# Performance work log

Hardware: AMD Instinct MI355X
Metric: run time of the kernel (lower is better)

Reference implementation:

```python
import jax, jax.numpy as jnp
import numpy as np

N = 8192      # num nodes
E = 8192      # num hyperedges
D = 256       # embedding dim
DENSITY = 0.01
LEAKY = 0.2   # negative_slope of LeakyReLU


def setup_inputs() -> dict:
    key = jax.random.key(0)
    k1, k2, k3, k4, k5 = jax.random.split(key, 5)
    # sparse adjacency matrices represented densely (values * bernoulli mask)
    inp_adj = jax.random.normal(k1, (E, N), dtype=jnp.float32) * (
        jax.random.uniform(k2, (E, N)) < DENSITY
    ).astype(jnp.float32)
    att_adj = jax.random.normal(k3, (N, E), dtype=jnp.float32) * (
        jax.random.uniform(k4, (N, E)) < DENSITY
    ).astype(jnp.float32)
    embs = jax.random.normal(k5, (N, D), dtype=jnp.float32)
    return {"inp_adj": inp_adj, "att_adj": att_adj, "embs": embs}


def reference(inp_adj, att_adj, embs):
    # adj = att_adj @ inp_adj  (spgemm in the original)  -> [N, N]
    adj = att_adj @ inp_adj
    # adj @ (adj.T @ embs)  (two spmm)  -> [N, D]
    out = adj @ (adj.T @ embs)
    # LeakyReLU(negative_slope=LEAKY)
    return jnp.where(out > 0, out, LEAKY * out)
```

## Files before the change

kernel.cpp:

```cpp
#include <hip/hip_runtime.h>
#include <stdint.h>

#define NROWS 8192
#define NCOLS 8192
#define DDIM  256
#define SLOTS 160
#define SCRN  192
#define CAP   786432

__device__ __forceinline__ float bf16lo(uint32_t u) { return __uint_as_float(u << 16); }
__device__ __forceinline__ float bf16hi(uint32_t u) { return __uint_as_float(u & 0xffff0000u); }
__device__ __forceinline__ uint32_t f2bf(float f) {
    uint32_t b = __float_as_uint(f);
    return (b + 0x7fffu + ((b >> 16) & 1u)) >> 16;
}

__global__ __launch_bounds__(256) void cvt_kernel(const float* __restrict__ in,
                                                  uint32_t* __restrict__ out) {
    int i = blockIdx.x * 256 + threadIdx.x;
    float2 f = ((const float2*)in)[i];
    out[i] = f2bf(f.x) | (f2bf(f.y) << 16);
}

__global__ __launch_bounds__(256) void zero_kernel(int* __restrict__ a,
                                                   int* __restrict__ b) {
    int i = blockIdx.x * 256 + threadIdx.x;
    a[i] = 0;
    b[i] = 0;
}

__device__ __forceinline__ void emit_nz(float v, uint32_t col, int& base,
                                        uint2* __restrict__ s) {
    unsigned long long m = __ballot(v != 0.f);
    if (m) {
        if (v != 0.f) {
            int pre = __builtin_amdgcn_mbcnt_hi((uint32_t)(m >> 32),
                      __builtin_amdgcn_mbcnt_lo((uint32_t)m, 0u));
            int o = base + pre;
            if (o < SCRN) s[o] = make_uint2(col, __float_as_uint(v));
        }
        base += (int)__popcll(m);
    }
}

template<int CH>
__device__ __forceinline__ void process_chunk(const float4 (&d)[8], int lane,
                                              int& base, uint2* __restrict__ s) {
    #pragma unroll
    for (int i = 0; i < 8; ++i) {
        const uint32_t cbase = (uint32_t)((CH * 512 + i * 64 + lane) * 4);
        emit_nz(d[i].x, cbase + 0, base, s);
        emit_nz(d[i].y, cbase + 1, base, s);
        emit_nz(d[i].z, cbase + 2, base, s);
        emit_nz(d[i].w, cbase + 3, base, s);
    }
}

__global__ __launch_bounds__(256) void extract_kernel(
        const float* __restrict__ M,
        int* __restrict__ rc, uint2* __restrict__ pair, int* __restrict__ ct) {
    __shared__ uint2 scr[4][SCRN];
    const int wv   = threadIdx.x >> 6;
    const int lane = threadIdx.x & 63;
    const int r = blockIdx.x * 4 + wv;

    const float4* __restrict__ M4 = (const float4*)(M + (size_t)r * NCOLS);
    uint2* __restrict__ dst = pair + (size_t)r * SLOTS;
    uint2* __restrict__ s = scr[wv];

    float4 da[8], db[8];
    #pragma unroll
    for (int i = 0; i < 8; ++i) da[i] = M4[0 * 512 + i * 64 + lane];
    #pragma unroll
    for (int i = 0; i < 8; ++i) db[i] = M4[1 * 512 + i * 64 + lane];
    __builtin_amdgcn_sched_barrier(0);

    int base = 0;
    process_chunk<0>(da, lane, base, s);
    #pragma unroll
    for (int i = 0; i < 8; ++i) da[i] = M4[2 * 512 + i * 64 + lane];
    __builtin_amdgcn_sched_barrier(0);
    process_chunk<1>(db, lane, base, s);
    #pragma unroll
    for (int i = 0; i < 8; ++i) db[i] = M4[3 * 512 + i * 64 + lane];
    __builtin_amdgcn_sched_barrier(0);
    process_chunk<2>(da, lane, base, s);
    process_chunk<3>(db, lane, base, s);

    const int n = base < SLOTS ? base : SLOTS;
    for (int j = lane; j < n; j += 64) {
        uint2 e = s[j];
        dst[j] = e;
        atomicAdd(&ct[e.x], 1);
    }
    if (lane == 0) rc[r] = n;
}

__global__ __launch_bounds__(256) void prefix_kernel(
        const int* __restrict__ totA, int* __restrict__ startA, int* __restrict__ curA,
        const int* __restrict__ totB, int* __restrict__ startB, int* __restrict__ curB) {
    const int* cnt = blockIdx.x ? totB : totA;
    int* start     = blockIdx.x ? startB : startA;
    int* cur       = blockIdx.x ? curB : curA;
    __shared__ int wtot[4];
    const int tid = threadIdx.x;
    const int wv = tid >> 6, lane = tid & 63;
    const int chunk = NCOLS / 256;
    const int base = tid * chunk;
    int sum = 0;
    for (int i = 0; i < chunk; ++i) sum += cnt[base + i];
    int inc = sum;
    #pragma unroll
    for (int sd = 1; sd < 64; sd <<= 1) {
        int t = __shfl_up(inc, sd, 64);
        if (lane >= sd) inc += t;
    }
    if (lane == 63) wtot[wv] = inc;
    __syncthreads();
    if (tid == 0) {
        int acc = 0;
        #pragma unroll
        for (int i = 0; i < 4; ++i) { int t = wtot[i]; wtot[i] = acc; acc += t; }
    }
    __syncthreads();
    int run = wtot[wv] + inc - sum;
    for (int i = 0; i < chunk; ++i) {
        start[base + i] = run;
        cur[base + i]   = run;
        run += cnt[base + i];
    }
}

__global__ __launch_bounds__(256) void scatter_kernel(
        const int* __restrict__ rcA, const uint2* __restrict__ pairA,
        int* __restrict__ curA, uint2* __restrict__ cscA,
        const int* __restrict__ rcB, const uint2* __restrict__ pairB,
        int* __restrict__ curB, uint2* __restrict__ cscB) {
    const int wv   = threadIdx.x >> 6;
    const int lane = threadIdx.x & 63;
    const int W = blockIdx.x * 4 + wv;
    const int which = W >> 13;
    const int r = W & (NROWS - 1);
    const uint2* pair = which ? pairB : pairA;
    int* cur          = which ? curB : curA;
    uint2* csc        = which ? cscB : cscA;
    const int c = (which ? rcB : rcA)[r];
    const uint2* __restrict__ p = pair + (size_t)r * SLOTS;
    for (int j = lane; j < c; j += 64) {
        uint2 e = p[j];
        int slot = atomicAdd(&cur[e.x], 1);
        csc[slot] = make_uint2((uint32_t)r, e.y);
    }
}

struct Acc8 { float a0, a1, a2, a3, a4, a5, a6, a7; };

__device__ __forceinline__ void fma8(Acc8& a, float v, uint4 t) {
    a.a0 = fmaf(v, bf16lo(t.x), a.a0); a.a1 = fmaf(v, bf16hi(t.x), a.a1);
    a.a2 = fmaf(v, bf16lo(t.y), a.a2); a.a3 = fmaf(v, bf16hi(t.y), a.a3);
    a.a4 = fmaf(v, bf16lo(t.z), a.a4); a.a5 = fmaf(v, bf16hi(t.z), a.a5);
    a.a6 = fmaf(v, bf16lo(t.w), a.a6); a.a7 = fmaf(v, bf16hi(t.w), a.a7);
}

template<int FINAL>
__global__ __launch_bounds__(256) void spmm_kernel(
        const int* __restrict__ start, const int* __restrict__ cnt,
        const uint2* __restrict__ pairs,
        const uint4* __restrict__ X,
        void* __restrict__ Y, int fixed_stride) {
    const int wv   = threadIdx.x >> 6;
    const int lane = threadIdx.x & 63;
    const int half = lane >> 5, sub = lane & 31;
    const int r = blockIdx.x * 4 + wv;
    const int c = cnt[r];
    const uint2* __restrict__ P = pairs + (fixed_stride ? (size_t)r * SLOTS : (size_t)start[r]);
    Acc8 a = {0.f, 0.f, 0.f, 0.f, 0.f, 0.f, 0.f, 0.f};
    int j = 0;
    const int nfull = c >> 4;
    if (nfull > 0) {
        uint2 p[8];
        #pragma unroll
        for (int t = 0; t < 8; ++t) p[t] = P[2 * t + half];
        for (int b = 0; b < nfull; ++b) {
            uint2 pn[8];
            if (b + 1 < nfull) {
                #pragma unroll
                for (int t = 0; t < 8; ++t) pn[t] = P[(b + 1) * 16 + 2 * t + half];
            }
            uint4 x[8];
            #pragma unroll
            for (int t = 0; t < 8; ++t) x[t] = X[(size_t)p[t].x * 32 + sub];
            #pragma unroll
            for (int t = 0; t < 8; ++t) fma8(a, __uint_as_float(p[t].y), x[t]);
            #pragma unroll
            for (int t = 0; t < 8; ++t) p[t] = pn[t];
        }
        j = nfull * 16;
    }
    for (; j + 1 < c; j += 2) {
        uint2 p = P[j + half];
        uint4 x = X[(size_t)p.x * 32 + sub];
        fma8(a, __uint_as_float(p.y), x);
    }
    if (j < c) {
        uint2 p = P[j];
        uint4 x = X[(size_t)p.x * 32 + sub];
        float v = half ? 0.f : __uint_as_float(p.y);
        fma8(a, v, x);
    }
    a.a0 += __shfl_xor(a.a0, 32); a.a1 += __shfl_xor(a.a1, 32);
    a.a2 += __shfl_xor(a.a2, 32); a.a3 += __shfl_xor(a.a3, 32);
    a.a4 += __shfl_xor(a.a4, 32); a.a5 += __shfl_xor(a.a5, 32);
    a.a6 += __shfl_xor(a.a6, 32); a.a7 += __shfl_xor(a.a7, 32);
    if (half == 0) {
        if (FINAL) {
            a.a0 = a.a0 > 0.f ? a.a0 : 0.2f * a.a0; a.a1 = a.a1 > 0.f ? a.a1 : 0.2f * a.a1;
            a.a2 = a.a2 > 0.f ? a.a2 : 0.2f * a.a2; a.a3 = a.a3 > 0.f ? a.a3 : 0.2f * a.a3;
            a.a4 = a.a4 > 0.f ? a.a4 : 0.2f * a.a4; a.a5 = a.a5 > 0.f ? a.a5 : 0.2f * a.a5;
            a.a6 = a.a6 > 0.f ? a.a6 : 0.2f * a.a6; a.a7 = a.a7 > 0.f ? a.a7 : 0.2f * a.a7;
            float4* Y4 = (float4*)Y;
            Y4[(size_t)r * 64 + sub * 2]     = make_float4(a.a0, a.a1, a.a2, a.a3);
            Y4[(size_t)r * 64 + sub * 2 + 1] = make_float4(a.a4, a.a5, a.a6, a.a7);
        } else {
            uint4 o;
            o.x = f2bf(a.a0) | (f2bf(a.a1) << 16);
            o.y = f2bf(a.a2) | (f2bf(a.a3) << 16);
            o.z = f2bf(a.a4) | (f2bf(a.a5) << 16);
            o.w = f2bf(a.a6) | (f2bf(a.a7) << 16);
            ((uint4*)Y)[(size_t)r * 32 + sub] = o;
        }
    }
}

extern "C" void kernel_launch(void* const* d_in, const int* in_sizes, int n_in,
                              void* d_out, int out_size, void* d_ws, size_t ws_size,
                              hipStream_t stream) {
    const float* Bm   = (const float*)d_in[0];
    const float* Am   = (const float*)d_in[1];
    const float* embs = (const float*)d_in[2];
    float* out = (float*)d_out;

    char* w = (char*)d_ws;
    auto alloc = [&](size_t bytes) -> char* {
        char* p = w;
        w += (bytes + 255) & ~(size_t)255;
        return p;
    };
    uint32_t* embs16 = (uint32_t*)alloc((size_t)NROWS * DDIM * 2);
    uint32_t* t1     = (uint32_t*)alloc((size_t)NROWS * DDIM * 2);
    uint32_t* t2     = (uint32_t*)alloc((size_t)NROWS * DDIM * 2);
    uint32_t* t3     = t1;

    int* rcA       = (int*)alloc(NROWS * 4);
    int* rcB       = (int*)alloc(NROWS * 4);
    int* coltotA   = (int*)alloc(NCOLS * 4);
    int* colstartA = (int*)alloc(NCOLS * 4);
    int* curA      = (int*)alloc(NCOLS * 4);
    int* coltotB   = (int*)alloc(NCOLS * 4);
    int* colstartB = (int*)alloc(NCOLS * 4);
    int* curB      = (int*)alloc(NCOLS * 4);

    uint2* csrA = (uint2*)alloc((size_t)NROWS * SLOTS * 8);
    uint2* csrB = (uint2*)alloc((size_t)NROWS * SLOTS * 8);
    uint2* cscA = (uint2*)alloc((size_t)CAP * 8);
    uint2* cscB = (uint2*)alloc((size_t)CAP * 8);

    zero_kernel<<<32, 256, 0, stream>>>(coltotA, coltotB);
    cvt_kernel<<<(NROWS * DDIM / 2) / 256, 256, 0, stream>>>(embs, embs16);
    extract_kernel<<<NROWS / 4, 256, 0, stream>>>(Am, rcA, csrA, coltotA);
    extract_kernel<<<NROWS / 4, 256, 0, stream>>>(Bm, rcB, csrB, coltotB);
    prefix_kernel<<<2, 256, 0, stream>>>(coltotA, colstartA, curA,
                                         coltotB, colstartB, curB);
    scatter_kernel<<<2 * NROWS / 4, 256, 0, stream>>>(rcA, csrA, curA, cscA,
                                                      rcB, csrB, curB, cscB);
    spmm_kernel<0><<<NROWS / 4, 256, 0, stream>>>(colstartA, coltotA, cscA, (const uint4*)embs16, t1, 0);
    spmm_kernel<0><<<NROWS / 4, 256, 0, stream>>>(colstartB, coltotB, cscB, (const uint4*)t1, t2, 0);
    spmm_kernel<0><<<NROWS / 4, 256, 0, stream>>>(nullptr, rcB, csrB, (const uint4*)t2, t3, 1);
    spmm_kernel<1><<<NROWS / 4, 256, 0, stream>>>(nullptr, rcA, csrA, (const uint4*)t3, out, 1);

    (void)in_sizes; (void)n_in; (void)out_size; (void)ws_size;
}
```

Measured before the change: 712.0 us.

## Fuse scatter and four SpMM stages into one persistent kernel with grid barriers

Measured after the change: 1.220 ms. +71.3%, slower.

```diff
diff --git a/kernel.cpp b/kernel.cpp
--- a/kernel.cpp
+++ b/kernel.cpp
@@ -7,6 +7,8 @@
 #define SLOTS 160
 #define SCRN  192
 #define CAP   786432
+#define MBLK  1024
+#define MWAVE (MBLK * 4)
 
 __device__ __forceinline__ float bf16lo(uint32_t u) { return __uint_as_float(u << 16); }
 __device__ __forceinline__ float bf16hi(uint32_t u) { return __uint_as_float(u & 0xffff0000u); }
@@ -23,10 +25,12 @@
 }
 
 __global__ __launch_bounds__(256) void zero_kernel(int* __restrict__ a,
-                                                   int* __restrict__ b) {
+                                                   int* __restrict__ b,
+                                                   int* __restrict__ bar) {
     int i = blockIdx.x * 256 + threadIdx.x;
     a[i] = 0;
     b[i] = 0;
+    if (i == 0) bar[0] = 0;
 }
 
 __device__ __forceinline__ void emit_nz(float v, uint32_t col, int& base,
@@ -131,28 +135,6 @@
     }
 }
 
-__global__ __launch_bounds__(256) void scatter_kernel(
-        const int* __restrict__ rcA, const uint2* __restrict__ pairA,
-        int* __restrict__ curA, uint2* __restrict__ cscA,
-        const int* __restrict__ rcB, const uint2* __restrict__ pairB,
-        int* __restrict__ curB, uint2* __restrict__ cscB) {
-    const int wv   = threadIdx.x >> 6;
-    const int lane = threadIdx.x & 63;
-    const int W = blockIdx.x * 4 + wv;
-    const int which = W >> 13;
-    const int r = W & (NROWS - 1);
-    const uint2* pair = which ? pairB : pairA;
-    int* cur          = which ? curB : curA;
-    uint2* csc        = which ? cscB : cscA;
-    const int c = (which ? rcB : rcA)[r];
-    const uint2* __restrict__ p = pair + (size_t)r * SLOTS;
-    for (int j = lane; j < c; j += 64) {
-        uint2 e = p[j];
-        int slot = atomicAdd(&cur[e.x], 1);
-        csc[slot] = make_uint2((uint32_t)r, e.y);
-    }
-}
-
 struct Acc8 { float a0, a1, a2, a3, a4, a5, a6, a7; };
 
 __device__ __forceinline__ void fma8(Acc8& a, float v, uint4 t) {
@@ -163,39 +145,24 @@
 }
 
 template<int FINAL>
-__global__ __launch_bounds__(256) void spmm_kernel(
+__device__ __forceinline__ void spmm_row(
         const int* __restrict__ start, const int* __restrict__ cnt,
-        const uint2* __restrict__ pairs,
-        const uint4* __restrict__ X,
-        void* __restrict__ Y, int fixed_stride) {
-    const int wv   = threadIdx.x >> 6;
-    const int lane = threadIdx.x & 63;
+        const uint2* __restrict__ pairs, const uint4* __restrict__ X,
+        void* __restrict__ Y, int fixed_stride, int r, int lane) {
     const int half = lane >> 5, sub = lane & 31;
-    const int r = blockIdx.x * 4 + wv;
     const int c = cnt[r];
     const uint2* __restrict__ P = pairs + (fixed_stride ? (size_t)r * SLOTS : (size_t)start[r]);
     Acc8 a = {0.f, 0.f, 0.f, 0.f, 0.f, 0.f, 0.f, 0.f};
     int j = 0;
-    const int nfull = c >> 4;
-    if (nfull > 0) {
+    for (; j + 15 < c; j += 16) {
         uint2 p[8];
+        uint4 x[8];
         #pragma unroll
-        for (int t = 0; t < 8; ++t) p[t] = P[2 * t + half];
-        for (int b = 0; b < nfull; ++b) {
-            uint2 pn[8];
-            if (b + 1 < nfull) {
-                #pragma unroll
-                for (int t = 0; t < 8; ++t) pn[t] = P[(b + 1) * 16 + 2 * t + half];
-            }
-            uint4 x[8];
-            #pragma unroll
-            for (int t = 0; t < 8; ++t) x[t] = X[(size_t)p[t].x * 32 + sub];
-            #pragma unroll
-            for (int t = 0; t < 8; ++t) fma8(a, __uint_as_float(p[t].y), x[t]);
-            #pragma unroll
-            for (int t = 0; t < 8; ++t) p[t] = pn[t];
-        }
-        j = nfull * 16;
+        for (int t = 0; t < 8; ++t) p[t] = P[j + 2 * t + half];
+        #pragma unroll
+        for (int t = 0; t < 8; ++t) x[t] = X[(size_t)p[t].x * 32 + sub];
+        #pragma unroll
+        for (int t = 0; t < 8; ++t) fma8(a, __uint_as_float(p[t].y), x[t]);
     }
     for (; j + 1 < c; j += 2) {
         uint2 p = P[j + half];
@@ -232,6 +199,59 @@
     }
 }
 
+__device__ __forceinline__ void gridbar(int* __restrict__ bar, int target) {
+    __syncthreads();
+    if (threadIdx.x == 0) {
+        __threadfence();
+        atomicAdd(bar, 1);
+        while (atomicAdd(bar, 0) < target) __builtin_amdgcn_s_sleep(8);
+        __threadfence();
+    }
+    __syncthreads();
+}
+
+__global__ __launch_bounds__(256, 4) void mega_kernel(
+        const int* __restrict__ rcA, const uint2* __restrict__ csrA,
+        int* __restrict__ curA, uint2* __restrict__ cscA,
+        const int* __restrict__ rcB, const uint2* __restrict__ csrB,
+        int* __restrict__ curB, uint2* __restrict__ cscB,
+        const int* __restrict__ colstartA, const int* __restrict__ coltotA,
+        const int* __restrict__ colstartB, const int* __restrict__ coltotB,
+        const uint4* __restrict__ embs16, uint32_t* __restrict__ t1,
+        uint32_t* __restrict__ t2, float* __restrict__ out,
+        int* __restrict__ bar) {
+    const int wv   = threadIdx.x >> 6;
+    const int lane = threadIdx.x & 63;
+    const int gw = blockIdx.x * 4 + wv;
+
+    for (int u = gw; u < 2 * NROWS; u += MWAVE) {
+        const int which = u >> 13;
+        const int r = u & (NROWS - 1);
+        const uint2* pair = which ? csrB : csrA;
+        int* cur          = which ? curB : curA;
+        uint2* csc        = which ? cscB : cscA;
+        const int c = (which ? rcB : rcA)[r];
+        const uint2* __restrict__ p = pair + (size_t)r * SLOTS;
+        for (int j = lane; j < c; j += 64) {
+            uint2 e = p[j];
+            int slot = atomicAdd(&cur[e.x], 1);
+            csc[slot] = make_uint2((uint32_t)r, e.y);
+        }
+    }
+    gridbar(bar, 1 * MBLK);
+    for (int r = gw; r < NROWS; r += MWAVE)
+        spmm_row<0>(colstartA, coltotA, cscA, embs16, t1, 0, r, lane);
+    gridbar(bar, 2 * MBLK);
+    for (int r = gw; r < NROWS; r += MWAVE)
+        spmm_row<0>(colstartB, coltotB, cscB, (const uint4*)t1, t2, 0, r, lane);
+    gridbar(bar, 3 * MBLK);
+    for (int r = gw; r < NROWS; r += MWAVE)
+        spmm_row<0>(nullptr, rcB, csrB, (const uint4*)t2, t1, 1, r, lane);
+    gridbar(bar, 4 * MBLK);
+    for (int r = gw; r < NROWS; r += MWAVE)
+        spmm_row<1>(nullptr, rcA, csrA, (const uint4*)t1, out, 1, r, lane);
+}
+
 extern "C" void kernel_launch(void* const* d_in, const int* in_sizes, int n_in,
                               void* d_out, int out_size, void* d_ws, size_t ws_size,
                               hipStream_t stream) {
@@ -249,7 +269,6 @@
     uint32_t* embs16 = (uint32_t*)alloc((size_t)NROWS * DDIM * 2);
     uint32_t* t1     = (uint32_t*)alloc((size_t)NROWS * DDIM * 2);
     uint32_t* t2     = (uint32_t*)alloc((size_t)NROWS * DDIM * 2);
-    uint32_t* t3     = t1;
 
     int* rcA       = (int*)alloc(NROWS * 4);
     int* rcB       = (int*)alloc(NROWS * 4);
@@ -259,24 +278,24 @@
     int* coltotB   = (int*)alloc(NCOLS * 4);
     int* colstartB = (int*)alloc(NCOLS * 4);
     int* curB      = (int*)alloc(NCOLS * 4);
+    int* bar       = (int*)alloc(256);
 
     uint2* csrA = (uint2*)alloc((size_t)NROWS * SLOTS * 8);
     uint2* csrB = (uint2*)alloc((size_t)NROWS * SLOTS * 8);
     uint2* cscA = (uint2*)alloc((size_t)CAP * 8);
     uint2* cscB = (uint2*)alloc((size_t)CAP * 8);
 
-    zero_kernel<<<32, 256, 0, stream>>>(coltotA, coltotB);
+    zero_kernel<<<32, 256, 0, stream>>>(coltotA, coltotB, bar);
     cvt_kernel<<<(NROWS * DDIM / 2) / 256, 256, 0, stream>>>(embs, embs16);
     extract_kernel<<<NROWS / 4, 256, 0, stream>>>(Am, rcA, csrA, coltotA);
     extract_kernel<<<NROWS / 4, 256, 0, stream>>>(Bm, rcB, csrB, coltotB);
     prefix_kernel<<<2, 256, 0, stream>>>(coltotA, colstartA, curA,
                                          coltotB, colstartB, curB);
-    scatter_kernel<<<2 * NROWS / 4, 256, 0, stream>>>(rcA, csrA, curA, cscA,
-                                                      rcB, csrB, curB, cscB);
-    spmm_kernel<0><<<NROWS / 4, 256, 0, stream>>>(colstartA, coltotA, cscA, (const uint4*)embs16, t1, 0);
-    spmm_kernel<0><<<NROWS / 4, 256, 0, stream>>>(colstartB, coltotB, cscB, (const uint4*)t1, t2, 0);
-    spmm_kernel<0><<<NROWS / 4, 256, 0, stream>>>(nullptr, rcB, csrB, (const uint4*)t2, t3, 1);
-    spmm_kernel<1><<<NROWS / 4, 256, 0, stream>>>(nullptr, rcA, csrA, (const uint4*)t3, out, 1);
+    mega_kernel<<<MBLK, 256, 0, stream>>>(rcA, csrA, curA, cscA,
+                                          rcB, csrB, curB, cscB,
+                                          colstartA, coltotA,
+                                          colstartB, coltotB,
+                                          (const uint4*)embs16, t1, t2, out, bar);
 
     (void)in_sizes; (void)n_in; (void)out_size; (void)ws_size;
 }
```
